# Performance work log

Hardware: AMD Instinct MI355X
Metric: run time of the kernel (lower is better)

Reference implementation:

```python
import jax, jax.numpy as jnp
import numpy as np

D = 1024
H = 16
DK = D // H
HID = 4096
EPS = 1e-5


def setup_inputs() -> dict:
    key = jax.random.key(0)
    ks = jax.random.split(key, 16)
    B, S = 2, 2048
    sc = lambda fan_in: 1.0 / np.sqrt(fan_in)
    inp = {
        "x": jax.random.normal(ks[0], (B, S, D), jnp.float32),
        "y": jax.random.normal(ks[1], (B, S, D), jnp.float32),
        "mask": jnp.ones((B, 1, 1, S), jnp.int32),
        # attention projections, stored [in, out]
        "Wq": jax.random.normal(ks[2], (D, D), jnp.float32) * sc(D),
        "bq": jnp.zeros((D,), jnp.float32),
        "Wk": jax.random.normal(ks[3], (D, D), jnp.float32) * sc(D),
        "bk": jnp.zeros((D,), jnp.float32),
        "Wv": jax.random.normal(ks[4], (D, D), jnp.float32) * sc(D),
        "bv": jnp.zeros((D,), jnp.float32),
        "Wo": jax.random.normal(ks[5], (D, D), jnp.float32) * sc(D),
        "bo": jnp.zeros((D,), jnp.float32),
        # FFN
        "W1": jax.random.normal(ks[6], (D, HID), jnp.float32) * sc(D),
        "b1": jnp.zeros((HID,), jnp.float32),
        "W2": jax.random.normal(ks[7], (HID, D), jnp.float32) * sc(HID),
        "b2": jnp.zeros((D,), jnp.float32),
        # LayerNorms
        "g1": jnp.ones((D,), jnp.float32),
        "be1": jnp.zeros((D,), jnp.float32),
        "g2": jnp.ones((D,), jnp.float32),
        "be2": jnp.zeros((D,), jnp.float32),
    }
    return inp


def _layer_norm(x, g, b):
    m = jnp.mean(x, axis=-1, keepdims=True)
    v = jnp.mean(jnp.square(x - m), axis=-1, keepdims=True)
    return (x - m) * jax.lax.rsqrt(v + EPS) * g + b


def _split_heads(t):  # [B,S,D] -> [B,H,S,DK]
    B, S, _ = t.shape
    return t.reshape(B, S, H, DK).transpose(0, 2, 1, 3)


def reference(x, y, mask, Wq, bq, Wk, bk, Wv, bv, Wo, bo,
              W1, b1, W2, b2, g1, be1, g2, be2):
    scale = 1.0 / np.sqrt(DK)
    Q = _split_heads(x @ Wq + bq)
    K = _split_heads(y @ Wk + bk)
    V = _split_heads(y @ Wv + bv)
    scores = jnp.einsum("bhqd,bhkd->bhqk", Q, K) * scale  # [B,H,S,S]
    scores = jnp.where(mask == 0, jnp.float32(-1e9), scores)
    probs = jax.nn.softmax(scores, axis=-1)
    attn = jnp.einsum("bhqk,bhkd->bhqd", probs, V)
    B, _, S, _ = attn.shape
    attn = attn.transpose(0, 2, 1, 3).reshape(B, S, D)
    mha_out = attn @ Wo + bo
    x1 = _layer_norm(x + mha_out, g1, be1)
    ff = jax.nn.relu(x1 @ W1 + b1) @ W2 + b2
    return _layer_norm(x1 + ff, g2, be2)
```

## Files before the change

kernel.cpp:

```cpp
#include <hip/hip_runtime.h>

#define S_ 2048
#define D_ 1024
#define B_ 2
#define H_ 16
#define DK_ 64
#define HID_ 4096

typedef unsigned short u16;
typedef __attribute__((ext_vector_type(8))) short short8;
typedef __attribute__((ext_vector_type(4))) float f32x4;

__device__ __forceinline__ float bf2f(u16 u) {
  return __uint_as_float(((unsigned int)u) << 16);
}
__device__ __forceinline__ u16 f2bf(float f) {
  unsigned int x = __float_as_uint(f);
  x += 0x7fff + ((x >> 16) & 1);
  return (u16)(x >> 16);
}

__global__ __launch_bounds__(256) void cvt_f2b(const float* __restrict__ in, u16* __restrict__ outp) {
  const int i = blockIdx.x * 256 + threadIdx.x;
  float4 v = ((const float4*)in)[i];
  unsigned int lo = (unsigned int)f2bf(v.x) | ((unsigned int)f2bf(v.y) << 16);
  unsigned int hi = (unsigned int)f2bf(v.z) | ((unsigned int)f2bf(v.w) << 16);
  ((uint2*)outp)[i] = make_uint2(lo, hi);
}

template<int MT, int NT, int OUTF32>
__global__ __launch_bounds__(256) void gemm_bt(
    const u16* __restrict__ A, const u16* __restrict__ Bt,
    const float* __restrict__ bias, void* __restrict__ Cv,
    int K, int lda, int ldb, int ldc,
    long sA, long sB, long sC, int relu) {
  constexpr int BM = MT * 32;
  constexpr int BN = NT * 32;
  __shared__ __align__(16) u16 As[BM * 32];
  __shared__ __align__(16) u16 Bs[BN * 32];
  const int z = blockIdx.z;
  A  += (long)z * sA;
  Bt += (long)z * sB;
  const int tid  = threadIdx.x;
  const int lane = tid & 63, wave = tid >> 6;
  const int quad = lane >> 4, l15 = lane & 15;
  const int wm = wave >> 1, wn = wave & 1;
  const u16* Ab = A  + (long)(blockIdx.y * BM) * lda;
  const u16* Bb = Bt + (long)(blockIdx.x * BN) * ldb;

  f32x4 acc[MT][NT];
#pragma unroll
  for (int i = 0; i < MT; ++i)
#pragma unroll
    for (int j = 0; j < NT; ++j) acc[i][j] = (f32x4){0.f, 0.f, 0.f, 0.f};

  const int r0  = tid >> 2;
  const int kk0 = (tid & 3) * 8;

  for (int kt = 0; kt < K; kt += 32) {
#pragma unroll
    for (int p = 0; p < BM / 64; ++p) {
      __builtin_amdgcn_global_load_lds(
          (const __attribute__((address_space(1))) void*)(Ab + (long)(p * 64 + r0) * lda + kt + kk0),
          (__attribute__((address_space(3))) void*)(&As[p * 2048 + tid * 8]), 16, 0, 0);
    }
#pragma unroll
    for (int p = 0; p < BN / 64; ++p) {
      __builtin_amdgcn_global_load_lds(
          (const __attribute__((address_space(1))) void*)(Bb + (long)(p * 64 + r0) * ldb + kt + kk0),
          (__attribute__((address_space(3))) void*)(&Bs[p * 2048 + tid * 8]), 16, 0, 0);
    }
    __syncthreads();
    short8 af[MT], bfr[NT];
#pragma unroll
    for (int mt = 0; mt < MT; ++mt)
      af[mt] = *(const short8*)&As[(wm * (MT * 16) + mt * 16 + l15) * 32 + quad * 8];
#pragma unroll
    for (int nt = 0; nt < NT; ++nt)
      bfr[nt] = *(const short8*)&Bs[(wn * (NT * 16) + nt * 16 + l15) * 32 + quad * 8];
#pragma unroll
    for (int mt = 0; mt < MT; ++mt)
#pragma unroll
      for (int nt = 0; nt < NT; ++nt)
        acc[mt][nt] = __builtin_amdgcn_mfma_f32_16x16x32_bf16(af[mt], bfr[nt], acc[mt][nt], 0, 0, 0);
    __syncthreads();
  }

#pragma unroll
  for (int nt = 0; nt < NT; ++nt) {
    const int col = blockIdx.x * BN + wn * (NT * 16) + nt * 16 + l15;
    const float bvv = bias ? bias[col] : 0.f;
#pragma unroll
    for (int mt = 0; mt < MT; ++mt) {
#pragma unroll
      for (int r = 0; r < 4; ++r) {
        const int row = blockIdx.y * BM + wm * (MT * 16) + mt * 16 + quad * 4 + r;
        float v = acc[mt][nt][r] + bvv;
        if (relu) v = fmaxf(v, 0.f);
        if (OUTF32) ((float*)Cv)[(long)z * sC + (long)row * ldc + col] = v;
        else        ((u16*)Cv)[(long)z * sC + (long)row * ldc + col] = f2bf(v);
      }
    }
  }
}

__global__ __launch_bounds__(256) void qkv_k(
    const u16* __restrict__ xb, const u16* __restrict__ yb,
    const u16* __restrict__ WqT, const u16* __restrict__ WkT, const u16* __restrict__ WvT,
    const float* __restrict__ bq, const float* __restrict__ bk, const float* __restrict__ bv,
    u16* __restrict__ Q, u16* __restrict__ Kp, u16* __restrict__ Vp) {
  __shared__ __align__(16) u16 As[128 * 32];
  __shared__ __align__(16) u16 Bs[128 * 32];
  const int z = blockIdx.z;
  const u16* A  = (z == 0) ? xb : yb;
  const u16* Bt = (z == 0) ? WqT : (z == 1) ? WkT : WvT;
  const float* bias = (z == 0) ? bq : (z == 1) ? bk : bv;
  u16* C = (z == 0) ? Q : (z == 1) ? Kp : Vp;
  const int tid  = threadIdx.x;
  const int lane = tid & 63, wave = tid >> 6;
  const int quad = lane >> 4, l15 = lane & 15;
  const int wm = wave >> 1, wn = wave & 1;
  const u16* Ab = A  + (long)(blockIdx.y * 128) * D_;
  const u16* Bb = Bt + (long)(blockIdx.x * 128) * D_;

  f32x4 acc[4][4];
#pragma unroll
  for (int i = 0; i < 4; ++i)
#pragma unroll
    for (int j = 0; j < 4; ++j) acc[i][j] = (f32x4){0.f, 0.f, 0.f, 0.f};

  const int r0  = tid >> 2;
  const int kk0 = (tid & 3) * 8;

  for (int kt = 0; kt < D_; kt += 32) {
#pragma unroll
    for (int p = 0; p < 2; ++p) {
      __builtin_amdgcn_global_load_lds(
          (const __attribute__((address_space(1))) void*)(Ab + (long)(p * 64 + r0) * D_ + kt + kk0),
          (__attribute__((address_space(3))) void*)(&As[p * 2048 + tid * 8]), 16, 0, 0);
      __builtin_amdgcn_global_load_lds(
          (const __attribute__((address_space(1))) void*)(Bb + (long)(p * 64 + r0) * D_ + kt + kk0),
          (__attribute__((address_space(3))) void*)(&Bs[p * 2048 + tid * 8]), 16, 0, 0);
    }
    __syncthreads();
    short8 af[4], bfr[4];
#pragma unroll
    for (int mt = 0; mt < 4; ++mt)
      af[mt] = *(const short8*)&As[(wm * 64 + mt * 16 + l15) * 32 + quad * 8];
#pragma unroll
    for (int nt = 0; nt < 4; ++nt)
      bfr[nt] = *(const short8*)&Bs[(wn * 64 + nt * 16 + l15) * 32 + quad * 8];
#pragma unroll
    for (int mt = 0; mt < 4; ++mt)
#pragma unroll
      for (int nt = 0; nt < 4; ++nt)
        acc[mt][nt] = __builtin_amdgcn_mfma_f32_16x16x32_bf16(af[mt], bfr[nt], acc[mt][nt], 0, 0, 0);
    __syncthreads();
  }

#pragma unroll
  for (int nt = 0; nt < 4; ++nt) {
    const int col = blockIdx.x * 128 + wn * 64 + nt * 16 + l15;
    const float bvv = bias[col];
#pragma unroll
    for (int mt = 0; mt < 4; ++mt) {
#pragma unroll
      for (int r = 0; r < 4; ++r) {
        const int row = blockIdx.y * 128 + wm * 64 + mt * 16 + quad * 4 + r;
        C[(long)row * D_ + col] = f2bf(acc[mt][nt][r] + bvv);
      }
    }
  }
}

__global__ void transpose_k(const float* __restrict__ in, u16* __restrict__ outp, int R, int Ccols) {
  __shared__ u16 tile[32][33];
  const int c0 = blockIdx.x * 32, r0 = blockIdx.y * 32;
  const int tx = threadIdx.x, ty = threadIdx.y;
  for (int i = ty; i < 32; i += 8)
    tile[i][tx] = f2bf(in[(long)(r0 + i) * Ccols + c0 + tx]);
  __syncthreads();
  for (int i = ty; i < 32; i += 8)
    outp[(long)(c0 + i) * R + r0 + tx] = tile[tx][i];
}

__global__ void vtrans_k(const u16* __restrict__ V, u16* __restrict__ Vt) {
  __shared__ u16 tile[32][33];
  const int bh = blockIdx.z, b = bh >> 4, h = bh & 15;
  const u16* in = V + (long)b * S_ * D_ + h * DK_;
  u16* outp = Vt + (long)bh * DK_ * S_;
  const int s0 = blockIdx.x * 32, d0 = blockIdx.y * 32;
  const int tx = threadIdx.x, ty = threadIdx.y;
  for (int i = ty; i < 32; i += 8)
    tile[i][tx] = in[(long)(s0 + i) * D_ + d0 + tx];
  __syncthreads();
  for (int i = ty; i < 32; i += 8)
    outp[(long)(d0 + i) * S_ + s0 + tx] = tile[tx][i];
}

#define FA_LDS 151552
__global__ __launch_bounds__(512, 2) void flash_k(
    const u16* __restrict__ Q, const u16* __restrict__ Kp, const u16* __restrict__ Vt,
    const int* __restrict__ mask, u16* __restrict__ ctx) {
  extern __shared__ __align__(16) char smem[];
  u16*   sQ    = (u16*)(smem);
  u16*   sK    = (u16*)(smem + 36864);
  u16*   sV    = (u16*)(smem + 55296);
  u16*   sP    = (u16*)(smem + 72704);
  float* sBias = (float*)(smem + 142336);
  float* sL    = (float*)(smem + 150528);

  const int qt = blockIdx.x, bh = blockIdx.y;
  const int b = bh >> 4, h = bh & 15;
  const int qbase = qt * 256;
  const int tid = threadIdx.x;
  const int w = tid >> 6, lane = tid & 63;
  const int quad = lane >> 4, l15 = lane & 15;

  const u16* Qg  = Q  + ((long)b * S_ + qbase) * D_ + h * DK_;
  const u16* Kg  = Kp + (long)b * S_ * D_ + h * DK_;
  const u16* Vtg = Vt + (long)bh * DK_ * S_;
  u16* ctxg = ctx + ((long)b * S_ + qbase) * D_ + h * DK_;

#pragma unroll
  for (int p = 0; p < 4; ++p) {
    const int idx = p * 512 + tid;
    const int row = idx >> 3, cb = idx & 7;
    uint4 v = *(const uint4*)(Qg + (long)row * D_ + cb * 8);
    *(uint4*)&sQ[row * 72 + cb * 8] = v;
  }
  {
    int4 mv = ((const int4*)(mask + (long)b * S_))[tid];
    sBias[tid * 4 + 0] = mv.x ? 0.f : -1e30f;
    sBias[tid * 4 + 1] = mv.y ? 0.f : -1e30f;
    sBias[tid * 4 + 2] = mv.z ? 0.f : -1e30f;
    sBias[tid * 4 + 3] = mv.w ? 0.f : -1e30f;
  }

  uint4 kreg[2], vreg[2];
  const int krow = tid >> 3, kcb = tid & 7;
  const int vd = tid >> 4, vcb = tid & 15;
#pragma unroll
  for (int p = 0; p < 2; ++p) {
    kreg[p] = *(const uint4*)(Kg  + (long)(p * 64 + krow) * D_ + kcb * 8);
    vreg[p] = *(const uint4*)(Vtg + (long)(p * 32 + vd) * S_ + vcb * 8);
  }

  float lsum[2] = {0.f, 0.f};
  f32x4 accO[2][4];
#pragma unroll
  for (int i = 0; i < 2; ++i)
#pragma unroll
    for (int j = 0; j < 4; ++j) accO[i][j] = (f32x4){0.f, 0.f, 0.f, 0.f};

  for (int t = 0; t < 16; ++t) {
#pragma unroll
    for (int p = 0; p < 2; ++p) {
      *(uint4*)&sK[(p * 64 + krow) * 72 + kcb * 8] = kreg[p];
      *(uint4*)&sV[(p * 32 + vd) * 136 + vcb * 8] = vreg[p];
    }
    __syncthreads();
    if (t < 15) {
      const int kb2 = (t + 1) * 128;
#pragma unroll
      for (int p = 0; p < 2; ++p) {
        kreg[p] = *(const uint4*)(Kg  + (long)(kb2 + p * 64 + krow) * D_ + kcb * 8);
        vreg[p] = *(const uint4*)(Vtg + (long)(p * 32 + vd) * S_ + kb2 + vcb * 8);
      }
    }
    f32x4 accS[8][2];
#pragma unroll
    for (int i = 0; i < 8; ++i)
#pragma unroll
      for (int j = 0; j < 2; ++j) accS[i][j] = (f32x4){0.f, 0.f, 0.f, 0.f};
#pragma unroll
    for (int kt = 0; kt < 2; ++kt) {
      short8 kf[8], qf[2];
#pragma unroll
      for (int mt = 0; mt < 8; ++mt)
        kf[mt] = *(const short8*)&sK[(mt * 16 + l15) * 72 + kt * 32 + quad * 8];
#pragma unroll
      for (int nt = 0; nt < 2; ++nt)
        qf[nt] = *(const short8*)&sQ[(w * 32 + nt * 16 + l15) * 72 + kt * 32 + quad * 8];
#pragma unroll
      for (int mt = 0; mt < 8; ++mt)
#pragma unroll
        for (int nt = 0; nt < 2; ++nt)
          accS[mt][nt] = __builtin_amdgcn_mfma_f32_16x16x32_bf16(kf[mt], qf[nt], accS[mt][nt], 0, 0, 0);
    }
#pragma unroll
    for (int mt = 0; mt < 8; ++mt) {
      const f32x4 b4 = *(const f32x4*)&sBias[t * 128 + mt * 16 + quad * 4];
#pragma unroll
      for (int nt = 0; nt < 2; ++nt) {
#pragma unroll
        for (int r = 0; r < 4; ++r) {
          float s = accS[mt][nt][r] * 0.125f + b4[r];
          s = fminf(s, 30.f);
          const float p = __expf(s);
          accS[mt][nt][r] = p;
          lsum[nt] += p;
        }
        const int q = w * 32 + nt * 16 + l15;
        ushort4 pk;
        pk.x = f2bf(accS[mt][nt][0]); pk.y = f2bf(accS[mt][nt][1]);
        pk.z = f2bf(accS[mt][nt][2]); pk.w = f2bf(accS[mt][nt][3]);
        *(ushort4*)&sP[q * 136 + mt * 16 + quad * 4] = pk;
      }
    }
#pragma unroll
    for (int kt = 0; kt < 4; ++kt) {
      short8 pf[2], vf[4];
#pragma unroll
      for (int mt = 0; mt < 2; ++mt)
        pf[mt] = *(const short8*)&sP[(w * 32 + mt * 16 + l15) * 136 + kt * 32 + quad * 8];
#pragma unroll
      for (int nt = 0; nt < 4; ++nt)
        vf[nt] = *(const short8*)&sV[(nt * 16 + l15) * 136 + kt * 32 + quad * 8];
#pragma unroll
      for (int mt = 0; mt < 2; ++mt)
#pragma unroll
        for (int nt = 0; nt < 4; ++nt)
          accO[mt][nt] = __builtin_amdgcn_mfma_f32_16x16x32_bf16(pf[mt], vf[nt], accO[mt][nt], 0, 0, 0);
    }
    __syncthreads();
  }

#pragma unroll
  for (int nt = 0; nt < 2; ++nt) {
    float l = lsum[nt];
    l += __shfl_xor(l, 16, 64);
    l += __shfl_xor(l, 32, 64);
    if (quad == 0) sL[w * 32 + nt * 16 + l15] = l;
  }
#pragma unroll
  for (int mt = 0; mt < 2; ++mt) {
    const f32x4 rl = *(const f32x4*)&sL[w * 32 + mt * 16 + quad * 4];
#pragma unroll
    for (int nt = 0; nt < 4; ++nt) {
#pragma unroll
      for (int r = 0; r < 4; ++r) {
        const float o = accO[mt][nt][r] / rl[r];
        ctxg[(long)(w * 32 + mt * 16 + quad * 4 + r) * D_ + nt * 16 + l15] = f2bf(o);
      }
    }
  }
}

__device__ __forceinline__ float block_reduce_sum(float v, float* red) {
#pragma unroll
  for (int off = 32; off; off >>= 1) v += __shfl_down(v, off, 64);
  __syncthreads();
  if ((threadIdx.x & 63) == 0) red[threadIdx.x >> 6] = v;
  __syncthreads();
  return red[0] + red[1] + red[2] + red[3];
}

__global__ __launch_bounds__(256) void addln_fb(const float* __restrict__ A, const u16* __restrict__ Bres,
    const float* __restrict__ g, const float* __restrict__ be, u16* __restrict__ outp) {
  __shared__ float red[4];
  const int row = blockIdx.x, tid = threadIdx.x;
  const float4 av = ((const float4*)(A + (long)row * D_))[tid];
  const uint2 bv2 = ((const uint2*)(Bres + (long)row * D_))[tid];
  float xv[4];
  xv[0] = av.x + bf2f((u16)(bv2.x & 0xffff));
  xv[1] = av.y + bf2f((u16)(bv2.x >> 16));
  xv[2] = av.z + bf2f((u16)(bv2.y & 0xffff));
  xv[3] = av.w + bf2f((u16)(bv2.y >> 16));
  float s  = xv[0] + xv[1] + xv[2] + xv[3];
  float ss = xv[0]*xv[0] + xv[1]*xv[1] + xv[2]*xv[2] + xv[3]*xv[3];
  s  = block_reduce_sum(s, red);
  ss = block_reduce_sum(ss, red);
  const float m   = s * (1.0f / 1024.0f);
  const float var = ss * (1.0f / 1024.0f) - m * m;
  const float rs  = rsqrtf(var + 1e-5f);
  const int c0 = tid * 4;
  float v0 = (xv[0] - m) * rs * g[c0 + 0] + be[c0 + 0];
  float v1 = (xv[1] - m) * rs * g[c0 + 1] + be[c0 + 1];
  float v2 = (xv[2] - m) * rs * g[c0 + 2] + be[c0 + 2];
  float v3 = (xv[3] - m) * rs * g[c0 + 3] + be[c0 + 3];
  unsigned int o01 = (unsigned int)f2bf(v0) | ((unsigned int)f2bf(v1) << 16);
  unsigned int o23 = (unsigned int)f2bf(v2) | ((unsigned int)f2bf(v3) << 16);
  ((uint2*)(outp + (long)row * D_))[tid] = make_uint2(o01, o23);
}

__global__ __launch_bounds__(256) void addln2_bf(const u16* __restrict__ A,
    const float* __restrict__ p0, const float* __restrict__ p1, const float* __restrict__ b2,
    const float* __restrict__ g, const float* __restrict__ be, float* __restrict__ outp) {
  __shared__ float red[4];
  const int row = blockIdx.x, tid = threadIdx.x;
  const uint2 av  = ((const uint2*)(A + (long)row * D_))[tid];
  const float4 P0 = ((const float4*)(p0 + (long)row * D_))[tid];
  const float4 P1 = ((const float4*)(p1 + (long)row * D_))[tid];
  const int c0 = tid * 4;
  float xv[4];
  xv[0] = bf2f((u16)(av.x & 0xffff)) + P0.x + P1.x + b2[c0 + 0];
  xv[1] = bf2f((u16)(av.x >> 16))    + P0.y + P1.y + b2[c0 + 1];
  xv[2] = bf2f((u16)(av.y & 0xffff)) + P0.z + P1.z + b2[c0 + 2];
  xv[3] = bf2f((u16)(av.y >> 16))    + P0.w + P1.w + b2[c0 + 3];
  float s  = xv[0] + xv[1] + xv[2] + xv[3];
  float ss = xv[0]*xv[0] + xv[1]*xv[1] + xv[2]*xv[2] + xv[3]*xv[3];
  s  = block_reduce_sum(s, red);
  ss = block_reduce_sum(ss, red);
  const float m   = s * (1.0f / 1024.0f);
  const float var = ss * (1.0f / 1024.0f) - m * m;
  const float rs  = rsqrtf(var + 1e-5f);
  float4 o;
  o.x = (xv[0] - m) * rs * g[c0 + 0] + be[c0 + 0];
  o.y = (xv[1] - m) * rs * g[c0 + 1] + be[c0 + 1];
  o.z = (xv[2] - m) * rs * g[c0 + 2] + be[c0 + 2];
  o.w = (xv[3] - m) * rs * g[c0 + 3] + be[c0 + 3];
  ((float4*)(outp + (long)row * D_))[tid] = o;
}

extern "C" void kernel_launch(void* const* d_in, const int* in_sizes, int n_in,
                              void* d_out, int out_size, void* d_ws, size_t ws_size,
                              hipStream_t stream) {
  const float* x   = (const float*)d_in[0];
  const float* y   = (const float*)d_in[1];
  const int* mask  = (const int*)d_in[2];
  const float* Wq = (const float*)d_in[3];  const float* bq = (const float*)d_in[4];
  const float* Wk = (const float*)d_in[5];  const float* bk = (const float*)d_in[6];
  const float* Wv = (const float*)d_in[7];  const float* bv = (const float*)d_in[8];
  const float* Wo = (const float*)d_in[9];  const float* bo = (const float*)d_in[10];
  const float* W1 = (const float*)d_in[11]; const float* b1 = (const float*)d_in[12];
  const float* W2 = (const float*)d_in[13]; const float* b2 = (const float*)d_in[14];
  const float* g1 = (const float*)d_in[15]; const float* be1 = (const float*)d_in[16];
  const float* g2 = (const float*)d_in[17]; const float* be2 = (const float*)d_in[18];
  float* out = (float*)d_out;

  char* w = (char*)d_ws;
  const size_t MB = 1024 * 1024;
  u16* WqT = (u16*)(w + 0 * MB);
  u16* WkT = (u16*)(w + 2 * MB);
  u16* WvT = (u16*)(w + 4 * MB);
  u16* WoT = (u16*)(w + 6 * MB);
  u16* W1T = (u16*)(w + 8 * MB);
  u16* W2T = (u16*)(w + 16 * MB);
  u16* xb  = (u16*)(w + 24 * MB);
  u16* yb  = (u16*)(w + 32 * MB);
  u16* Q   = (u16*)(w + 40 * MB);
  u16* Kp  = (u16*)(w + 48 * MB);
  u16* Vp  = (u16*)(w + 56 * MB);
  u16* Vt  = (u16*)(w + 64 * MB);
  u16* ctx = (u16*)(w + 72 * MB);
  u16* mha = (u16*)(w + 80 * MB);
  u16* x1  = (u16*)(w + 88 * MB);
  u16* h1  = (u16*)(w + 96 * MB);
  float* pK = (float*)(w + 40 * MB);

  static int shmem_set = 0;
  hipFuncSetAttribute((const void*)flash_k, hipFuncAttributeMaxDynamicSharedMemorySize, FA_LDS);
  (void)shmem_set;

  dim3 t328(32, 8);
  transpose_k<<<dim3(32, 32), t328, 0, stream>>>(Wq, WqT, 1024, 1024);
  transpose_k<<<dim3(32, 32), t328, 0, stream>>>(Wk, WkT, 1024, 1024);
  transpose_k<<<dim3(32, 32), t328, 0, stream>>>(Wv, WvT, 1024, 1024);
  transpose_k<<<dim3(32, 32), t328, 0, stream>>>(Wo, WoT, 1024, 1024);
  transpose_k<<<dim3(128, 32), t328, 0, stream>>>(W1, W1T, 1024, 4096);
  transpose_k<<<dim3(32, 128), t328, 0, stream>>>(W2, W2T, 4096, 1024);
  cvt_f2b<<<dim3(4096), 256, 0, stream>>>(x, xb);
  cvt_f2b<<<dim3(4096), 256, 0, stream>>>(y, yb);

  qkv_k<<<dim3(8, 32, 3), 256, 0, stream>>>(xb, yb, WqT, WkT, WvT, bq, bk, bv, Q, Kp, Vp);

  vtrans_k<<<dim3(64, 2, 32), t328, 0, stream>>>(Vp, Vt);

  flash_k<<<dim3(8, 32), 512, FA_LDS, stream>>>(Q, Kp, Vt, mask, ctx);

  gemm_bt<2, 4, 0><<<dim3(8, 64, 1), 256, 0, stream>>>(ctx, WoT, bo, mha,
      1024, 1024, 1024, 1024, 0, 0, 0, 0);
  addln_fb<<<dim3(4096), 256, 0, stream>>>(x, mha, g1, be1, x1);

  gemm_bt<4, 4, 0><<<dim3(32, 32, 1), 256, 0, stream>>>(x1, W1T, b1, h1,
      1024, 1024, 1024, 4096, 0, 0, 0, 1);
  gemm_bt<4, 4, 1><<<dim3(8, 32, 2), 256, 0, stream>>>(h1, W2T, nullptr, (void*)pK,
      2048, 4096, 4096, 1024, 2048, 2048, (long)4096 * 1024, 0);
  addln2_bf<<<dim3(4096), 256, 0, stream>>>(x1, pK, pK + (long)4096 * 1024, b2, g2, be2, out);
}
```

Baseline: 472.3 us.

## Restructure flash attention with register-resident Q, 32-key double-buffered tiles and swizzled LDS

Rewrites the attention kernel to use 256 threads with 64 query rows per wave. Q fragments are held in registers, keys are processed in double-buffered 32-key tiles, and the P tile uses an XOR-swizzled LDS layout to avoid bank conflicts. The softmax scale and log2(e) are folded into the Q projection so exp2f is used directly, and the mask bias is precomputed by a small separate kernel. It also cuts LDS from about 148KB to 64KB and swaps block index order so heads vary fastest. In exchange it loops over many more, smaller tiles with a barrier per tile, and bf16 rounding of the pre-scaled Q differs slightly.

```diff
diff --git a/kernel.cpp b/kernel.cpp
--- a/kernel.cpp
+++ b/kernel.cpp
@@ -19,6 +19,9 @@
   x += 0x7fff + ((x >> 16) & 1);
   return (u16)(x >> 16);
 }
+__device__ __forceinline__ unsigned int pk2bf(float lo, float hi) {
+  return ((__float_as_uint(lo) + 0x8000u) >> 16) | ((__float_as_uint(hi) + 0x8000u) & 0xffff0000u);
+}
 
 __global__ __launch_bounds__(256) void cvt_f2b(const float* __restrict__ in, u16* __restrict__ outp) {
   const int i = blockIdx.x * 256 + threadIdx.x;
@@ -26,6 +29,11 @@
   unsigned int lo = (unsigned int)f2bf(v.x) | ((unsigned int)f2bf(v.y) << 16);
   unsigned int hi = (unsigned int)f2bf(v.z) | ((unsigned int)f2bf(v.w) << 16);
   ((uint2*)outp)[i] = make_uint2(lo, hi);
+}
+
+__global__ __launch_bounds__(256) void maskbias_k(const int* __restrict__ mask, float* __restrict__ biasf) {
+  const int i = blockIdx.x * 256 + threadIdx.x;
+  biasf[i] = mask[i] ? 0.f : -1e30f;
 }
 
 template<int MT, int NT, int OUTF32>
@@ -116,6 +124,7 @@
   const u16* Bt = (z == 0) ? WqT : (z == 1) ? WkT : WvT;
   const float* bias = (z == 0) ? bq : (z == 1) ? bk : bv;
   u16* C = (z == 0) ? Q : (z == 1) ? Kp : Vp;
+  const float sc = (z == 0) ? 0.18033688011112042f : 1.0f;
   const int tid  = threadIdx.x;
   const int lane = tid & 63, wave = tid >> 6;
   const int quad = lane >> 4, l15 = lane & 15;
@@ -167,7 +176,7 @@
 #pragma unroll
       for (int r = 0; r < 4; ++r) {
         const int row = blockIdx.y * 128 + wm * 64 + mt * 16 + quad * 4 + r;
-        C[(long)row * D_ + col] = f2bf(acc[mt][nt][r] + bvv);
+        C[(long)row * D_ + col] = f2bf((acc[mt][nt][r] + bvv) * sc);
       }
     }
   }
@@ -198,151 +207,146 @@
     outp[(long)(d0 + i) * S_ + s0 + tx] = tile[tx][i];
 }
 
-#define FA_LDS 151552
-__global__ __launch_bounds__(512, 2) void flash_k(
+#define FA_LDS 65536
+__global__ __launch_bounds__(256, 2) void flash_k(
     const u16* __restrict__ Q, const u16* __restrict__ Kp, const u16* __restrict__ Vt,
-    const int* __restrict__ mask, u16* __restrict__ ctx) {
+    const float* __restrict__ biasf, u16* __restrict__ ctx) {
   extern __shared__ __align__(16) char smem[];
-  u16*   sQ    = (u16*)(smem);
-  u16*   sK    = (u16*)(smem + 36864);
-  u16*   sV    = (u16*)(smem + 55296);
-  u16*   sP    = (u16*)(smem + 72704);
-  float* sBias = (float*)(smem + 142336);
-  float* sL    = (float*)(smem + 150528);
-
-  const int qt = blockIdx.x, bh = blockIdx.y;
+  u16* sQ = (u16*)smem;
+  u16* sK = (u16*)(smem + 32768);
+  u16* sV = (u16*)(smem + 40960);
+  u16* sP = (u16*)(smem + 49152);
+
+  const int bh = blockIdx.x, qt = blockIdx.y;
   const int b = bh >> 4, h = bh & 15;
-  const int qbase = qt * 256;
   const int tid = threadIdx.x;
   const int w = tid >> 6, lane = tid & 63;
   const int quad = lane >> 4, l15 = lane & 15;
-
-  const u16* Qg  = Q  + ((long)b * S_ + qbase) * D_ + h * DK_;
+  const int swz = ((l15 ^ (l15 >> 2)) & 3) << 3;
+
+  const u16* Qg  = Q  + ((long)b * S_ + qt * 256) * D_ + h * DK_;
   const u16* Kg  = Kp + (long)b * S_ * D_ + h * DK_;
   const u16* Vtg = Vt + (long)bh * DK_ * S_;
-  u16* ctxg = ctx + ((long)b * S_ + qbase) * D_ + h * DK_;
-
-#pragma unroll
-  for (int p = 0; p < 4; ++p) {
-    const int idx = p * 512 + tid;
+  const float* biasg = biasf + b * S_;
+  u16* ctxg = ctx + ((long)b * S_ + qt * 256) * D_ + h * DK_;
+
+  const int krow = tid >> 3, kc = tid & 7;
+  const u16* kptr = Kg + (long)krow * D_ + kc * 8;
+  const int ksw = ((kc >> 2) << 10) + krow * 32 + (kc & 3) * 8;
+  const int vrow = tid >> 2, vc = tid & 3;
+  const u16* vptr = Vtg + (long)vrow * S_ + vc * 8;
+  const int vsw = vrow * 32 + vc * 8;
+
+  uint4 kreg = *(const uint4*)kptr;
+  uint4 vreg = *(const uint4*)vptr;
+
+#pragma unroll
+  for (int p = 0; p < 8; ++p) {
+    const int idx = p * 256 + tid;
     const int row = idx >> 3, cb = idx & 7;
     uint4 v = *(const uint4*)(Qg + (long)row * D_ + cb * 8);
-    *(uint4*)&sQ[row * 72 + cb * 8] = v;
-  }
-  {
-    int4 mv = ((const int4*)(mask + (long)b * S_))[tid];
-    sBias[tid * 4 + 0] = mv.x ? 0.f : -1e30f;
-    sBias[tid * 4 + 1] = mv.y ? 0.f : -1e30f;
-    sBias[tid * 4 + 2] = mv.z ? 0.f : -1e30f;
-    sBias[tid * 4 + 3] = mv.w ? 0.f : -1e30f;
-  }
-
-  uint4 kreg[2], vreg[2];
-  const int krow = tid >> 3, kcb = tid & 7;
-  const int vd = tid >> 4, vcb = tid & 15;
-#pragma unroll
-  for (int p = 0; p < 2; ++p) {
-    kreg[p] = *(const uint4*)(Kg  + (long)(p * 64 + krow) * D_ + kcb * 8);
-    vreg[p] = *(const uint4*)(Vtg + (long)(p * 32 + vd) * S_ + vcb * 8);
-  }
-
-  float lsum[2] = {0.f, 0.f};
-  f32x4 accO[2][4];
-#pragma unroll
-  for (int i = 0; i < 2; ++i)
+    *(uint4*)&sQ[(cb >> 2) * 8192 + row * 32 + (cb & 3) * 8] = v;
+  }
+  *(uint4*)&sK[ksw] = kreg;
+  *(uint4*)&sV[vsw] = vreg;
+  kreg = *(const uint4*)(kptr + 32 * D_);
+  vreg = *(const uint4*)(vptr + 32);
+  kptr += 64 * D_;
+  vptr += 64;
+  __syncthreads();
+
+  short8 qf[4][2];
+#pragma unroll
+  for (int nt = 0; nt < 4; ++nt)
+#pragma unroll
+    for (int kt = 0; kt < 2; ++kt)
+      qf[nt][kt] = *(const short8*)&sQ[kt * 8192 + (w * 64 + nt * 16 + l15) * 32 + quad * 8];
+
+  float lsum[4] = {0.f, 0.f, 0.f, 0.f};
+  f32x4 accO[4][4];
+#pragma unroll
+  for (int i = 0; i < 4; ++i)
 #pragma unroll
     for (int j = 0; j < 4; ++j) accO[i][j] = (f32x4){0.f, 0.f, 0.f, 0.f};
 
-  for (int t = 0; t < 16; ++t) {
-#pragma unroll
-    for (int p = 0; p < 2; ++p) {
-      *(uint4*)&sK[(p * 64 + krow) * 72 + kcb * 8] = kreg[p];
-      *(uint4*)&sV[(p * 32 + vd) * 136 + vcb * 8] = vreg[p];
-    }
-    __syncthreads();
-    if (t < 15) {
-      const int kb2 = (t + 1) * 128;
-#pragma unroll
-      for (int p = 0; p < 2; ++p) {
-        kreg[p] = *(const uint4*)(Kg  + (long)(kb2 + p * 64 + krow) * D_ + kcb * 8);
-        vreg[p] = *(const uint4*)(Vtg + (long)(p * 32 + vd) * S_ + kb2 + vcb * 8);
+  for (int t = 0; t < 64; ++t) {
+    if (t) __syncthreads();
+    const int buf = (t & 1) << 11;
+    const int nbuf = buf ^ 2048;
+    if (t < 63) {
+      *(uint4*)&sK[nbuf + ksw] = kreg;
+      *(uint4*)&sV[nbuf + vsw] = vreg;
+      if (t < 62) {
+        kreg = *(const uint4*)kptr;
+        vreg = *(const uint4*)vptr;
+        kptr += 32 * D_;
+        vptr += 32;
       }
     }
-    f32x4 accS[8][2];
-#pragma unroll
-    for (int i = 0; i < 8; ++i)
-#pragma unroll
-      for (int j = 0; j < 2; ++j) accS[i][j] = (f32x4){0.f, 0.f, 0.f, 0.f};
+    float4 bv0 = *(const float4*)(biasg + t * 32 + quad * 4);
+    float4 bv1 = *(const float4*)(biasg + t * 32 + 16 + quad * 4);
+
+    f32x4 accS[2][4];
+#pragma unroll
+    for (int i = 0; i < 2; ++i)
+#pragma unroll
+      for (int j = 0; j < 4; ++j) accS[i][j] = (f32x4){0.f, 0.f, 0.f, 0.f};
 #pragma unroll
     for (int kt = 0; kt < 2; ++kt) {
-      short8 kf[8], qf[2];
-#pragma unroll
-      for (int mt = 0; mt < 8; ++mt)
-        kf[mt] = *(const short8*)&sK[(mt * 16 + l15) * 72 + kt * 32 + quad * 8];
-#pragma unroll
-      for (int nt = 0; nt < 2; ++nt)
-        qf[nt] = *(const short8*)&sQ[(w * 32 + nt * 16 + l15) * 72 + kt * 32 + quad * 8];
-#pragma unroll
-      for (int mt = 0; mt < 8; ++mt)
-#pragma unroll
-        for (int nt = 0; nt < 2; ++nt)
-          accS[mt][nt] = __builtin_amdgcn_mfma_f32_16x16x32_bf16(kf[mt], qf[nt], accS[mt][nt], 0, 0, 0);
-    }
-#pragma unroll
-    for (int mt = 0; mt < 8; ++mt) {
-      const f32x4 b4 = *(const f32x4*)&sBias[t * 128 + mt * 16 + quad * 4];
-#pragma unroll
-      for (int nt = 0; nt < 2; ++nt) {
-#pragma unroll
-        for (int r = 0; r < 4; ++r) {
-          float s = accS[mt][nt][r] * 0.125f + b4[r];
-          s = fminf(s, 30.f);
-          const float p = __expf(s);
-          accS[mt][nt][r] = p;
-          lsum[nt] += p;
-        }
-        const int q = w * 32 + nt * 16 + l15;
-        ushort4 pk;
-        pk.x = f2bf(accS[mt][nt][0]); pk.y = f2bf(accS[mt][nt][1]);
-        pk.z = f2bf(accS[mt][nt][2]); pk.w = f2bf(accS[mt][nt][3]);
-        *(ushort4*)&sP[q * 136 + mt * 16 + quad * 4] = pk;
+      short8 kf0 = *(const short8*)&sK[buf + kt * 1024 + l15 * 32 + quad * 8];
+      short8 kf1 = *(const short8*)&sK[buf + kt * 1024 + (16 + l15) * 32 + quad * 8];
+#pragma unroll
+      for (int nt = 0; nt < 4; ++nt) {
+        accS[0][nt] = __builtin_amdgcn_mfma_f32_16x16x32_bf16(kf0, qf[nt][kt], accS[0][nt], 0, 0, 0);
+        accS[1][nt] = __builtin_amdgcn_mfma_f32_16x16x32_bf16(kf1, qf[nt][kt], accS[1][nt], 0, 0, 0);
       }
     }
 #pragma unroll
-    for (int kt = 0; kt < 4; ++kt) {
-      short8 pf[2], vf[4];
-#pragma unroll
-      for (int mt = 0; mt < 2; ++mt)
-        pf[mt] = *(const short8*)&sP[(w * 32 + mt * 16 + l15) * 136 + kt * 32 + quad * 8];
-#pragma unroll
-      for (int nt = 0; nt < 4; ++nt)
-        vf[nt] = *(const short8*)&sV[(nt * 16 + l15) * 136 + kt * 32 + quad * 8];
-#pragma unroll
-      for (int mt = 0; mt < 2; ++mt)
-#pragma unroll
-        for (int nt = 0; nt < 4; ++nt)
-          accO[mt][nt] = __builtin_amdgcn_mfma_f32_16x16x32_bf16(pf[mt], vf[nt], accO[mt][nt], 0, 0, 0);
-    }
-    __syncthreads();
-  }
-
-#pragma unroll
-  for (int nt = 0; nt < 2; ++nt) {
-    float l = lsum[nt];
-    l += __shfl_xor(l, 16, 64);
-    l += __shfl_xor(l, 32, 64);
-    if (quad == 0) sL[w * 32 + nt * 16 + l15] = l;
-  }
-#pragma unroll
-  for (int mt = 0; mt < 2; ++mt) {
-    const f32x4 rl = *(const f32x4*)&sL[w * 32 + mt * 16 + quad * 4];
-#pragma unroll
-    for (int nt = 0; nt < 4; ++nt) {
-#pragma unroll
-      for (int r = 0; r < 4; ++r) {
-        const float o = accO[mt][nt][r] / rl[r];
-        ctxg[(long)(w * 32 + mt * 16 + quad * 4 + r) * D_ + nt * 16 + l15] = f2bf(o);
+    for (int mt = 0; mt < 2; ++mt) {
+      const float4 bv = mt ? bv1 : bv0;
+      const int kvl = ((mt * 16 + quad * 4) ^ swz);
+#pragma unroll
+      for (int nt = 0; nt < 4; ++nt) {
+        float p0 = exp2f(fminf(accS[mt][nt][0] + bv.x, 30.f));
+        float p1 = exp2f(fminf(accS[mt][nt][1] + bv.y, 30.f));
+        float p2 = exp2f(fminf(accS[mt][nt][2] + bv.z, 30.f));
+        float p3 = exp2f(fminf(accS[mt][nt][3] + bv.w, 30.f));
+        lsum[nt] += (p0 + p1) + (p2 + p3);
+        *(uint2*)&sP[(w * 64 + nt * 16 + l15) * 32 + kvl] =
+            make_uint2(pk2bf(p0, p1), pk2bf(p2, p3));
       }
+    }
+    short8 pf[4], vf[4];
+#pragma unroll
+    for (int m = 0; m < 4; ++m)
+      pf[m] = *(const short8*)&sP[(w * 64 + m * 16 + l15) * 32 + ((quad * 8) ^ swz)];
+#pragma unroll
+    for (int n = 0; n < 4; ++n)
+      vf[n] = *(const short8*)&sV[buf + (n * 16 + l15) * 32 + quad * 8];
+#pragma unroll
+    for (int m = 0; m < 4; ++m)
+#pragma unroll
+      for (int n = 0; n < 4; ++n)
+        accO[m][n] = __builtin_amdgcn_mfma_f32_16x16x32_bf16(pf[m], vf[n], accO[m][n], 0, 0, 0);
+  }
+
+#pragma unroll
+  for (int nt = 0; nt < 4; ++nt) {
+    lsum[nt] += __shfl_xor(lsum[nt], 16, 64);
+    lsum[nt] += __shfl_xor(lsum[nt], 32, 64);
+  }
+#pragma unroll
+  for (int m = 0; m < 4; ++m) {
+    float inv[4];
+#pragma unroll
+    for (int r = 0; r < 4; ++r)
+      inv[r] = 1.f / __shfl(lsum[m], quad * 4 + r, 64);
+#pragma unroll
+    for (int n = 0; n < 4; ++n) {
+#pragma unroll
+      for (int r = 0; r < 4; ++r)
+        ctxg[(long)(w * 64 + m * 16 + quad * 4 + r) * D_ + n * 16 + l15] =
+            f2bf(accO[m][n][r] * inv[r]);
     }
   }
 }
@@ -448,10 +452,9 @@
   u16* x1  = (u16*)(w + 88 * MB);
   u16* h1  = (u16*)(w + 96 * MB);
   float* pK = (float*)(w + 40 * MB);
-
-  static int shmem_set = 0;
+  float* biasf = (float*)(w + 128 * MB);
+
   hipFuncSetAttribute((const void*)flash_k, hipFuncAttributeMaxDynamicSharedMemorySize, FA_LDS);
-  (void)shmem_set;
 
   dim3 t328(32, 8);
   transpose_k<<<dim3(32, 32), t328, 0, stream>>>(Wq, WqT, 1024, 1024);
@@ -462,12 +465,13 @@
   transpose_k<<<dim3(32, 128), t328, 0, stream>>>(W2, W2T, 4096, 1024);
   cvt_f2b<<<dim3(4096), 256, 0, stream>>>(x, xb);
   cvt_f2b<<<dim3(4096), 256, 0, stream>>>(y, yb);
+  maskbias_k<<<dim3(16), 256, 0, stream>>>(mask, biasf);
 
   qkv_k<<<dim3(8, 32, 3), 256, 0, stream>>>(xb, yb, WqT, WkT, WvT, bq, bk, bv, Q, Kp, Vp);
 
   vtrans_k<<<dim3(64, 2, 32), t328, 0, stream>>>(Vp, Vt);
 
-  flash_k<<<dim3(8, 32), 512, FA_LDS, stream>>>(Q, Kp, Vt, mask, ctx);
+  flash_k<<<dim3(32, 8), 256, FA_LDS, stream>>>(Q, Kp, Vt, biasf, ctx);
 
   gemm_bt<2, 4, 0><<<dim3(8, 64, 1), 256, 0, stream>>>(ctx, WoT, bo, mha,
       1024, 1024, 1024, 1024, 0, 0, 0, 0);
```

New measurement: 467.7 us. About the same (-1.0%).
